# Performance work log

Measured on AMD Instinct MI355X. Metric: run time of the kernel, lower is better.

Reference implementation:

```python
import jax, jax.numpy as jnp
import numpy as np
from jax.scipy.special import logsumexp

B, T, K = 256, 512, 20
START_TAG, STOP_TAG = 18, 19


def setup_inputs() -> dict:
    key = jax.random.key(0)
    k1, k2, k3, k4 = jax.random.split(key, 4)
    features = jax.random.normal(k1, (B, T, K, K), dtype=jnp.float32)
    transitions = jax.random.normal(k2, (K, K), dtype=jnp.float32)
    targets = jax.random.randint(k3, (B, T), 0, 18, dtype=jnp.int32)
    lengths = jax.random.randint(k4, (B,), 1, T + 1, dtype=jnp.int32)
    return {"features": features, "transitions": transitions,
            "targets": targets, "lengths": lengths}


def reference(features, transitions, targets, lengths):
    # features: [B, T, K, K] with features[b,t,i,j] = emission(tag i at t) + transition(j -> i)
    b, t, k, _ = features.shape
    valid = jnp.arange(t)[None, :] < lengths[:, None]  # [B, T]

    # ---- gold path score ----
    prev = jnp.concatenate(
        [jnp.full((b, 1), START_TAG, dtype=targets.dtype), targets[:, :-1]], axis=1)
    flat_idx = targets.astype(jnp.int32) * k + prev.astype(jnp.int32)  # [B, T]
    scores_at_targets = jnp.take_along_axis(
        features.reshape(b, t, k * k), flat_idx[:, :, None].astype(jnp.int32), axis=2)[..., 0]
    last_tag = jnp.take_along_axis(targets, (lengths - 1)[:, None].astype(jnp.int32), axis=1)[:, 0]
    gold_score = jnp.sum(jnp.where(valid, scores_at_targets, 0.0)) \
        + jnp.sum(transitions[STOP_TAG, last_tag])

    # ---- forward algorithm (sequential log-sum-exp scan over time) ----
    alpha0 = features[:, 0, :, START_TAG]  # [B, K]; all lengths >= 1

    def step(alpha, inp):
        f_t, tt = inp  # f_t: [B, K, K]
        new = logsumexp(f_t + alpha[:, None, :], axis=2)  # [B, K]
        active = (tt < lengths)[:, None]
        return jnp.where(active, new, alpha), None

    feats_rest = jnp.swapaxes(features[:, 1:], 0, 1)  # [T-1, B, K, K]
    alpha, _ = jax.lax.scan(step, alpha0, (feats_rest, jnp.arange(1, t)))

    all_paths_scores = jnp.sum(logsumexp(alpha + transitions[STOP_TAG][None, :], axis=1))
    return all_paths_scores - gold_score
```

## Files before the change

kernel.cpp:

```cpp
#include <hip/hip_runtime.h>
#include <math.h>
#include <stdint.h>

#define BB 256
#define TT 512
#define KK 20
#define START_TAG 18
#define STOP_TAG 19
#define NST 400
#define SEGSTRIDE 420
#define WS_SEG_OFF 1024

typedef __bf16 bf16x8 __attribute__((ext_vector_type(8)));
typedef float f32x16 __attribute__((ext_vector_type(16)));
typedef uint32_t u32x4 __attribute__((ext_vector_type(4)));

__device__ __forceinline__ float fexp2(float x){ float r; asm("v_exp_f32 %0, %1":"=v"(r):"v"(x)); return r; }
__device__ __forceinline__ float flog2(float x){ float r; asm("v_log_f32 %0, %1":"=v"(r):"v"(x)); return r; }
__device__ __forceinline__ uint32_t pk_bf16(float lo, float hi){
  uint32_t r; asm("v_cvt_pk_bf16_f32 %0, %1, %2":"=v"(r):"v"(lo),"v"(hi)); return r;
}
__device__ __forceinline__ void pswap(uint32_t &a, uint32_t &b){
  asm("v_permlane32_swap_b32 %0, %1":"+v"(a),"+v"(b));
}
__device__ __forceinline__ f32x16 mfma_bf16(u32x4 a, u32x4 b, f32x16 c){
  return __builtin_amdgcn_mfma_f32_32x32x16_bf16(
    __builtin_bit_cast(bf16x8,a), __builtin_bit_cast(bf16x8,b), c, 0,0,0);
}

template<int SEGL, int SEGS>
__global__ __launch_bounds__(64) void seg_mfma(
    const float* __restrict__ feats, const int* __restrict__ lengths,
    float* __restrict__ wseg)
{
  constexpr float LOG2E = 1.4426950408889634f;
  const int lane = threadIdx.x;
  const int n  = lane & 31;
  const int hi = lane >> 5;
  const int task = blockIdx.x;
  const int b = task / SEGS;
  const int s = task - b*SEGS;
  const int seg0 = 1 + SEGL*s;
  const int len = lengths[b];
  int nv = len - seg0; nv = nv < 0 ? 0 : (nv > SEGL ? SEGL : nv);
  if (nv <= 0) return;

  const bool rowok = n < KK;
  const int rli = rowok ? n : 0;
  const float* rbase = feats + (size_t)(b*TT + seg0)*NST + rli*KK;
  const int off0 = hi ? 8 : 0;

  u32x4 B0, B1;
  #pragma unroll
  for (int d=0; d<4; ++d){
    int k0 = hi*8 + 2*d;
    uint32_t v = 0;
    if (k0   == n && n < KK) v |= 0x3F80u;
    if (k0+1 == n && n < KK) v |= 0x3F800000u;
    B0[d] = v;
    int m0 = 16 + hi*8 + 2*d;
    uint32_t u = 0;
    if (m0   == n && n < KK) u |= 0x3F800000u * 0 + ((m0 == n && n < KK) ? 0x3F80u : 0u);
    u = 0;
    if (m0   == n && n < KK) u |= 0x3F80u;
    if (m0+1 == n && n < KK) u |= 0x3F800000u;
    B1[d] = u;
  }

  int cexp = 0;
  f32x16 acc;
  #pragma unroll
  for (int r=0;r<16;++r) acc[r] = 0.f;

  float4 a0,a1,a2, p0,p1,p2, q0,q1,q2;
  auto LD = [&](int it, float4 &r0, float4 &r1, float4 &r2){
    const float* p = rbase + (size_t)it*NST;
    r0 = *(const float4*)(p + off0);
    r1 = *(const float4*)(p + off0 + 4);
    r2 = (hi == 0) ? *(const float4*)(p + 16) : make_float4(0.f,0.f,0.f,0.f);
  };
  auto CONV = [&](const float4 &r0, const float4 &r1, const float4 &r2,
                  u32x4 &A0, u32x4 &A1){
    uint32_t w0 = pk_bf16(fexp2(r0.x*LOG2E), fexp2(r0.y*LOG2E));
    uint32_t w1 = pk_bf16(fexp2(r0.z*LOG2E), fexp2(r0.w*LOG2E));
    uint32_t w2 = pk_bf16(fexp2(r1.x*LOG2E), fexp2(r1.y*LOG2E));
    uint32_t w3 = pk_bf16(fexp2(r1.z*LOG2E), fexp2(r1.w*LOG2E));
    uint32_t w4 = pk_bf16(fexp2(r2.x*LOG2E), fexp2(r2.y*LOG2E));
    uint32_t w5 = pk_bf16(fexp2(r2.z*LOG2E), fexp2(r2.w*LOG2E));
    if (!rowok){ w0=0u; w1=0u; w2=0u; w3=0u; }
    if (!(rowok && hi==0)){ w4=0u; w5=0u; }
    A0[0]=w0; A0[1]=w1; A0[2]=w2; A0[3]=w3;
    A1[0]=w4; A1[1]=w5; A1[2]=0u; A1[3]=0u;
  };
  auto RENORM = [&](){
    float mx = acc[0];
    #pragma unroll
    for (int r=1;r<16;++r) mx = fmaxf(mx, acc[r]);
    mx = fmaxf(mx, __shfl_xor(mx, 32, 64));
    int e = (int)((__float_as_uint(mx) >> 23) & 255) - 127;
    if (e < -100) e = -100;
    float sc = __uint_as_float((uint32_t)(127 - e) << 23);
    #pragma unroll
    for (int r=0;r<16;++r) acc[r] *= sc;
    cexp += e;
  };
  auto C2B = [&](){
    uint32_t x0 = pk_bf16(acc[0],  acc[1]);
    uint32_t x1 = pk_bf16(acc[2],  acc[3]);
    uint32_t x2 = pk_bf16(acc[4],  acc[5]);
    uint32_t x3 = pk_bf16(acc[6],  acc[7]);
    uint32_t x4 = pk_bf16(acc[8],  acc[9]);
    uint32_t x5 = pk_bf16(acc[10], acc[11]);
    uint32_t x6 = pk_bf16(acc[12], acc[13]);
    uint32_t x7 = pk_bf16(acc[14], acc[15]);
    pswap(x0,x2); pswap(x1,x3); pswap(x4,x6); pswap(x5,x7);
    B0[0]=x0; B0[1]=x1; B0[2]=x2; B0[3]=x3;
    B1[0]=x4; B1[1]=x5; B1[2]=x6; B1[3]=x7;
  };

  LD(0, a0,a1,a2);
  LD((1 < nv) ? 1 : 0, p0,p1,p2);
  q0=a0; q1=a1; q2=a2;
  for (int it=0; it<nv; ++it){
    if (it+2 < nv) LD(it+2, q0,q1,q2);
    u32x4 A0, A1; CONV(a0,a1,a2, A0,A1);
    f32x16 z;
    #pragma unroll
    for (int r=0;r<16;++r) z[r] = 0.f;
    acc = mfma_bf16(A0, B0, z);
    acc = mfma_bf16(A1, B1, acc);
    if (it == nv-1) break;
    if ((it & 7) == 7) RENORM();
    C2B();
    a0=p0; a1=p1; a2=p2;
    p0=q0; p1=q1; p2=q2;
  }
  RENORM();

  float* out = wseg + (size_t)task*SEGSTRIDE;
  #pragma unroll
  for (int r=0;r<16;++r){
    int row = (r&3) + 8*(r>>2) + 4*hi;
    if (row < KK && n < KK) out[row*KK + n] = acc[r];
  }
  if (hi==0 && n<KK) ((int*)out)[NST + n] = cexp;
}

template<int SEGL, int SEGS>
__global__ __launch_bounds__(64,1) void chain_kernel2(
    const float* __restrict__ feats, const float* __restrict__ trans,
    const int* __restrict__ targets, const int* __restrict__ lengths,
    const float* __restrict__ wseg, float* __restrict__ partialA)
{
    constexpr float LOG2E = 1.4426950408889634f;
    constexpr float LN2   = 0.6931471805599453f;
    const int b = blockIdx.x;
    const int lane = threadIdx.x;
    const int len = lengths[b];
    const bool act = lane < KK;
    const int li = act ? lane : 0;

    __shared__ __align__(16) float Ul[KK];

    const float* fb = feats + (size_t)b*TT*NST;
    float a2 = fb[li*KK + START_TAG] * LOG2E;
    float c0 = __uint_as_float(__builtin_amdgcn_readfirstlane(__float_as_uint(a2)));
    float CW = c0;
    float wk = act ? fexp2(a2 - c0) : 0.f;

    const int nseg = (len - 1 + SEGL - 1) / SEGL;

    if (act && nseg > 0){
        float4 mA[5], mB[5];
        int cA = 0, cB = 0;
        auto LDM = [&](int s2, float4 (&m)[5], int& c){
            const float* base = wseg + (size_t)(b*SEGS + s2)*SEGSTRIDE;
            const float4* p4 = (const float4*)(base + li*KK);
            m[0]=p4[0]; m[1]=p4[1]; m[2]=p4[2]; m[3]=p4[3]; m[4]=p4[4];
            c = ((const int*)base)[NST + li];
        };
        auto STEP = [&](float4 (&m)[5], int c){
            int e = (int)((__float_as_uint(wk) >> 23) & 255) - 127;
            int q = __builtin_amdgcn_readfirstlane(c + e);
            Ul[li] = ldexpf(wk, c - q);
            asm volatile("s_waitcnt lgkmcnt(0)" ::: "memory");
            const float4* up = (const float4*)Ul;
            float4 u0 = up[0], u1 = up[1], u2 = up[2], u3 = up[3], u4 = up[4];
            float s0 = m[0].x*u0.x, s1 = m[0].y*u0.y;
            s0 = fmaf(m[0].z,u0.z,s0); s1 = fmaf(m[0].w,u0.w,s1);
            s0 = fmaf(m[1].x,u1.x,s0); s1 = fmaf(m[1].y,u1.y,s1);
            s0 = fmaf(m[1].z,u1.z,s0); s1 = fmaf(m[1].w,u1.w,s1);
            s0 = fmaf(m[2].x,u2.x,s0); s1 = fmaf(m[2].y,u2.y,s1);
            s0 = fmaf(m[2].z,u2.z,s0); s1 = fmaf(m[2].w,u2.w,s1);
            s0 = fmaf(m[3].x,u3.x,s0); s1 = fmaf(m[3].y,u3.y,s1);
            s0 = fmaf(m[3].z,u3.z,s0); s1 = fmaf(m[3].w,u3.w,s1);
            s0 = fmaf(m[4].x,u4.x,s0); s1 = fmaf(m[4].y,u4.y,s1);
            s0 = fmaf(m[4].z,u4.z,s0); s1 = fmaf(m[4].w,u4.w,s1);
            wk = s0 + s1;
            CW += (float)q;
            asm volatile("s_waitcnt lgkmcnt(0)" ::: "memory");
        };
        LDM(0, mA, cA);
        for (int s2 = 0; s2 < nseg; ){
            if (s2 + 1 < nseg) LDM(s2 + 1, mB, cB);
            STEP(mA, cA);
            ++s2; if (s2 >= nseg) break;
            if (s2 + 1 < nseg) LDM(s2 + 1, mA, cA);
            STEP(mB, cB);
            ++s2;
        }
    }

    float term = act ? wk * fexp2(trans[STOP_TAG*KK + li] * LOG2E) : 0.f;
    #pragma unroll
    for (int o = 32; o > 0; o >>= 1) term += __shfl_xor(term, o, 64);
    if (lane == 0){
        float lse = LN2 * (CW + flog2(term));
        int last = targets[b*TT + len - 1];
        partialA[b] = lse - trans[STOP_TAG*KK + last];
    }
}

__global__ __launch_bounds__(64,1) void fwd_serial(
    const float* __restrict__ feats, const float* __restrict__ trans,
    const int* __restrict__ targets, const int* __restrict__ lengths,
    float* __restrict__ partialA)
{
    constexpr float LOG2E = 1.4426950408889634f;
    constexpr float LN2   = 0.6931471805599453f;
    const int b    = blockIdx.x;
    const int lane = threadIdx.x;
    const int len  = lengths[b];
    const float* fb = feats + (size_t)b * TT * NST;
    __shared__ __align__(16) float alpha[KK];
    __shared__ __align__(16) float xs[KK];
    const bool act = lane < KK;
    const int  li  = act ? lane : 0;
    if (act) alpha[lane] = fb[lane * KK + START_TAG] * LOG2E;
    __syncthreads();
    float4 b0[5], b1[5], b2[5], b3[5];
    auto LOAD = [&](float4* dst, int t){
        int tc = (t < len) ? t : (len - 1);
        const float4* p = (const float4*)(fb + (size_t)tc * NST + li * KK);
        dst[0]=p[0]; dst[1]=p[1]; dst[2]=p[2]; dst[3]=p[3]; dst[4]=p[4];
    };
    auto STEP = [&](const float4* bufv){
        const float4* ap = (const float4*)alpha;
        float a[KK];
        #pragma unroll
        for (int q = 0; q < 5; ++q){
            float4 av = ap[q];
            a[4*q+0]=av.x; a[4*q+1]=av.y; a[4*q+2]=av.z; a[4*q+3]=av.w;
        }
        float v[KK];
        #pragma unroll
        for (int q = 0; q < 5; ++q){
            v[4*q+0] = bufv[q].x * LOG2E + a[4*q+0];
            v[4*q+1] = bufv[q].y * LOG2E + a[4*q+1];
            v[4*q+2] = bufv[q].z * LOG2E + a[4*q+2];
            v[4*q+3] = bufv[q].w * LOG2E + a[4*q+3];
        }
        float m = v[0];
        #pragma unroll
        for (int j = 1; j < KK; ++j) m = fmaxf(m, v[j]);
        float s = 0.f;
        #pragma unroll
        for (int j = 0; j < KK; ++j) s += fexp2(v[j] - m);
        float na = m + flog2(s);
        __syncthreads();
        if (act) alpha[lane] = na;
        __syncthreads();
    };
    LOAD(b0,1); LOAD(b1,2); LOAD(b2,3); LOAD(b3,4);
    int t = 1;
    while (t < len){
        STEP(b0); LOAD(b0, t+4); ++t; if (t >= len) break;
        STEP(b1); LOAD(b1, t+4); ++t; if (t >= len) break;
        STEP(b2); LOAD(b2, t+4); ++t; if (t >= len) break;
        STEP(b3); LOAD(b3, t+4); ++t;
    }
    if (act) xs[lane] = alpha[lane] + trans[STOP_TAG*KK + lane] * LOG2E;
    __syncthreads();
    if (lane == 0){
        float m = xs[0];
        for (int j = 1; j < KK; ++j) m = fmaxf(m, xs[j]);
        float s = 0.f;
        for (int j = 0; j < KK; ++j) s += fexp2(xs[j] - m);
        float lse = LN2 * (m + flog2(s));
        int last_tag = targets[b*TT + (len-1)];
        partialA[b] = lse - trans[STOP_TAG*KK + last_tag];
    }
}

__global__ __launch_bounds__(256) void gold_kernel(
    const float* __restrict__ feats, const int* __restrict__ targets,
    const int* __restrict__ lengths, float* __restrict__ partialG)
{
    const int b   = blockIdx.x;
    const int tt  = blockIdx.y * 256 + threadIdx.x;
    const int len = lengths[b];
    float val = 0.f;
    if (tt < len){
        int tgt  = targets[b*TT + tt];
        int prev = (tt > 0) ? targets[b*TT + tt - 1] : START_TAG;
        val = feats[((size_t)b*TT + tt)*NST + tgt*KK + prev];
    }
    #pragma unroll
    for (int off = 32; off > 0; off >>= 1) val += __shfl_down(val, off);
    __shared__ float wsum[4];
    if ((threadIdx.x & 63) == 0) wsum[threadIdx.x >> 6] = val;
    __syncthreads();
    if (threadIdx.x == 0)
        partialG[b*gridDim.y + blockIdx.y] = wsum[0]+wsum[1]+wsum[2]+wsum[3];
}

__global__ __launch_bounds__(256) void final_kernel(
    const float* __restrict__ partialA, const float* __restrict__ partialG,
    float* __restrict__ out)
{
    int tid = threadIdx.x;
    float v = partialA[tid] - partialG[tid] - partialG[tid + 256];
    #pragma unroll
    for (int off = 32; off > 0; off >>= 1) v += __shfl_down(v, off);
    __shared__ float wsum[4];
    if ((tid & 63) == 0) wsum[tid >> 6] = v;
    __syncthreads();
    if (tid == 0) out[0] = wsum[0]+wsum[1]+wsum[2]+wsum[3];
}

extern "C" void kernel_launch(void* const* d_in, const int* in_sizes, int n_in,
                              void* d_out, int out_size, void* d_ws, size_t ws_size,
                              hipStream_t stream) {
    const float* feats   = (const float*)d_in[0];
    const float* trans   = (const float*)d_in[1];
    const int*   targets = (const int*)d_in[2];
    const int*   lengths = (const int*)d_in[3];

    float* ws       = (float*)d_ws;
    float* partialA = ws;
    float* partialG = ws + 256;
    float* wseg     = ws + WS_SEG_OFF;

    const size_t need64 = (size_t)(WS_SEG_OFF + (size_t)BB*8*SEGSTRIDE) * sizeof(float);

    if (ws_size >= need64){
        seg_mfma<64,8><<<dim3(BB*8), dim3(64), 0, stream>>>(feats, lengths, wseg);
        chain_kernel2<64,8><<<dim3(BB), dim3(64), 0, stream>>>(feats, trans, targets, lengths, wseg, partialA);
    } else {
        fwd_serial<<<dim3(BB), dim3(64), 0, stream>>>(feats, trans, targets, lengths, partialA);
    }
    gold_kernel<<<dim3(BB, 2), dim3(256), 0, stream>>>(feats, targets, lengths, partialG);
    final_kernel<<<dim3(1), dim3(256), 0, stream>>>(partialA, partialG, (float*)d_out);
}
```

Before: 48.83 us.

## Fuse gold-path scoring into segment MFMA kernel and deepen load prefetch

The gold-path gather moves into seg_mfma, which already reads each feature row, so the separate gold_kernel pass over features is gone. Per-segment partial gold sums are written to partialG and reduced in a new templated final kernel. The t=0 gold term is added in chain_kernel2. The load pipeline also goes from a three-deep rotation to a four-deep manual unroll, at the cost of more registers, extra target loads and select logic per step.

```diff
diff --git a/kernel.cpp b/kernel.cpp
--- a/kernel.cpp
+++ b/kernel.cpp
@@ -9,7 +9,7 @@
 #define STOP_TAG 19
 #define NST 400
 #define SEGSTRIDE 420
-#define WS_SEG_OFF 1024
+#define WS_SEG_OFF 4096
 
 typedef __bf16 bf16x8 __attribute__((ext_vector_type(8)));
 typedef float f32x16 __attribute__((ext_vector_type(16)));
@@ -30,8 +30,9 @@
 
 template<int SEGL, int SEGS>
 __global__ __launch_bounds__(64) void seg_mfma(
-    const float* __restrict__ feats, const int* __restrict__ lengths,
-    float* __restrict__ wseg)
+    const float* __restrict__ feats, const int* __restrict__ targets,
+    const int* __restrict__ lengths, float* __restrict__ wseg,
+    float* __restrict__ partialG)
 {
   constexpr float LOG2E = 1.4426950408889634f;
   const int lane = threadIdx.x;
@@ -43,12 +44,13 @@
   const int seg0 = 1 + SEGL*s;
   const int len = lengths[b];
   int nv = len - seg0; nv = nv < 0 ? 0 : (nv > SEGL ? SEGL : nv);
-  if (nv <= 0) return;
+  if (nv <= 0){ if (lane == 0) partialG[task] = 0.f; return; }
 
   const bool rowok = n < KK;
   const int rli = rowok ? n : 0;
   const float* rbase = feats + (size_t)(b*TT + seg0)*NST + rli*KK;
   const int off0 = hi ? 8 : 0;
+  const int bT = b*TT;
 
   u32x4 B0, B1;
   #pragma unroll
@@ -60,27 +62,47 @@
     B0[d] = v;
     int m0 = 16 + hi*8 + 2*d;
     uint32_t u = 0;
-    if (m0   == n && n < KK) u |= 0x3F800000u * 0 + ((m0 == n && n < KK) ? 0x3F80u : 0u);
-    u = 0;
     if (m0   == n && n < KK) u |= 0x3F80u;
     if (m0+1 == n && n < KK) u |= 0x3F800000u;
     B1[d] = u;
   }
 
   int cexp = 0;
+  float gold = 0.f;
   f32x16 acc;
   #pragma unroll
   for (int r=0;r<16;++r) acc[r] = 0.f;
 
-  float4 a0,a1,a2, p0,p1,p2, q0,q1,q2;
-  auto LD = [&](int it, float4 &r0, float4 &r1, float4 &r2){
+  auto LDr = [&](int it, float4 &r0, float4 &r1, float4 &r2){
     const float* p = rbase + (size_t)it*NST;
     r0 = *(const float4*)(p + off0);
     r1 = *(const float4*)(p + off0 + 4);
     r2 = (hi == 0) ? *(const float4*)(p + 16) : make_float4(0.f,0.f,0.f,0.f);
   };
-  auto CONV = [&](const float4 &r0, const float4 &r1, const float4 &r2,
-                  u32x4 &A0, u32x4 &A1){
+
+  auto RENORM = [&](){
+    float mx = acc[0];
+    #pragma unroll
+    for (int r=1;r<16;++r) mx = fmaxf(mx, acc[r]);
+    mx = fmaxf(mx, __shfl_xor(mx, 32, 64));
+    int e = (int)((__float_as_uint(mx) >> 23) & 255) - 127;
+    if (e < -100) e = -100;
+    float sc = __uint_as_float((uint32_t)(127 - e) << 23);
+    #pragma unroll
+    for (int r=0;r<16;++r) acc[r] *= sc;
+    cexp += e;
+  };
+
+  auto BODY = [&](float4 &r0, float4 &r1, float4 &r2, int it){
+    int t   = seg0 + it;
+    int tgt = targets[bT + t];
+    int prv = targets[bT + t - 1];
+    int hsel = (prv >= 8 && prv < 16) ? 1 : 0;
+    int rsel = (prv >= 16) ? 2 : (((prv & 7) >= 4) ? 1 : 0);
+    int comp = prv & 3;
+    float4 rr = (rsel == 0) ? r0 : ((rsel == 1) ? r1 : r2);
+    float vv = (comp==0)?rr.x:((comp==1)?rr.y:((comp==2)?rr.z:rr.w));
+    if (n == tgt && hi == hsel) gold += vv;
     uint32_t w0 = pk_bf16(fexp2(r0.x*LOG2E), fexp2(r0.y*LOG2E));
     uint32_t w1 = pk_bf16(fexp2(r0.z*LOG2E), fexp2(r0.w*LOG2E));
     uint32_t w2 = pk_bf16(fexp2(r1.x*LOG2E), fexp2(r1.y*LOG2E));
@@ -89,51 +111,41 @@
     uint32_t w5 = pk_bf16(fexp2(r2.z*LOG2E), fexp2(r2.w*LOG2E));
     if (!rowok){ w0=0u; w1=0u; w2=0u; w3=0u; }
     if (!(rowok && hi==0)){ w4=0u; w5=0u; }
+    u32x4 A0, A1;
     A0[0]=w0; A0[1]=w1; A0[2]=w2; A0[3]=w3;
     A1[0]=w4; A1[1]=w5; A1[2]=0u; A1[3]=0u;
-  };
-  auto RENORM = [&](){
-    float mx = acc[0];
-    #pragma unroll
-    for (int r=1;r<16;++r) mx = fmaxf(mx, acc[r]);
-    mx = fmaxf(mx, __shfl_xor(mx, 32, 64));
-    int e = (int)((__float_as_uint(mx) >> 23) & 255) - 127;
-    if (e < -100) e = -100;
-    float sc = __uint_as_float((uint32_t)(127 - e) << 23);
-    #pragma unroll
-    for (int r=0;r<16;++r) acc[r] *= sc;
-    cexp += e;
-  };
-  auto C2B = [&](){
-    uint32_t x0 = pk_bf16(acc[0],  acc[1]);
-    uint32_t x1 = pk_bf16(acc[2],  acc[3]);
-    uint32_t x2 = pk_bf16(acc[4],  acc[5]);
-    uint32_t x3 = pk_bf16(acc[6],  acc[7]);
-    uint32_t x4 = pk_bf16(acc[8],  acc[9]);
-    uint32_t x5 = pk_bf16(acc[10], acc[11]);
-    uint32_t x6 = pk_bf16(acc[12], acc[13]);
-    uint32_t x7 = pk_bf16(acc[14], acc[15]);
-    pswap(x0,x2); pswap(x1,x3); pswap(x4,x6); pswap(x5,x7);
-    B0[0]=x0; B0[1]=x1; B0[2]=x2; B0[3]=x3;
-    B1[0]=x4; B1[1]=x5; B1[2]=x6; B1[3]=x7;
-  };
-
-  LD(0, a0,a1,a2);
-  LD((1 < nv) ? 1 : 0, p0,p1,p2);
-  q0=a0; q1=a1; q2=a2;
-  for (int it=0; it<nv; ++it){
-    if (it+2 < nv) LD(it+2, q0,q1,q2);
-    u32x4 A0, A1; CONV(a0,a1,a2, A0,A1);
     f32x16 z;
     #pragma unroll
     for (int r=0;r<16;++r) z[r] = 0.f;
     acc = mfma_bf16(A0, B0, z);
     acc = mfma_bf16(A1, B1, acc);
-    if (it == nv-1) break;
-    if ((it & 7) == 7) RENORM();
-    C2B();
-    a0=p0; a1=p1; a2=p2;
-    p0=q0; p1=q1; p2=q2;
+    if (it != nv-1){
+      if ((it & 7) == 7) RENORM();
+      uint32_t x0 = pk_bf16(acc[0],  acc[1]);
+      uint32_t x1 = pk_bf16(acc[2],  acc[3]);
+      uint32_t x2 = pk_bf16(acc[4],  acc[5]);
+      uint32_t x3 = pk_bf16(acc[6],  acc[7]);
+      uint32_t x4 = pk_bf16(acc[8],  acc[9]);
+      uint32_t x5 = pk_bf16(acc[10], acc[11]);
+      uint32_t x6 = pk_bf16(acc[12], acc[13]);
+      uint32_t x7 = pk_bf16(acc[14], acc[15]);
+      pswap(x0,x2); pswap(x1,x3); pswap(x4,x6); pswap(x5,x7);
+      B0[0]=x0; B0[1]=x1; B0[2]=x2; B0[3]=x3;
+      B1[0]=x4; B1[1]=x5; B1[2]=x6; B1[3]=x7;
+    }
+  };
+
+  float4 a0,a1,a2, b0,b1,b2, c0,c1,c2, d0,d1,d2;
+  LDr(0, a0,a1,a2);
+  if (1 < nv) LDr(1, b0,b1,b2);
+  if (2 < nv) LDr(2, c0,c1,c2);
+  if (3 < nv) LDr(3, d0,d1,d2);
+  int it = 0;
+  while (true){
+    BODY(a0,a1,a2, it); if (it+4 < nv) LDr(it+4, a0,a1,a2); if (++it >= nv) break;
+    BODY(b0,b1,b2, it); if (it+4 < nv) LDr(it+4, b0,b1,b2); if (++it >= nv) break;
+    BODY(c0,c1,c2, it); if (it+4 < nv) LDr(it+4, c0,c1,c2); if (++it >= nv) break;
+    BODY(d0,d1,d2, it); if (it+4 < nv) LDr(it+4, d0,d1,d2); if (++it >= nv) break;
   }
   RENORM();
 
@@ -144,6 +156,10 @@
     if (row < KK && n < KK) out[row*KK + n] = acc[r];
   }
   if (hi==0 && n<KK) ((int*)out)[NST + n] = cexp;
+
+  #pragma unroll
+  for (int o = 32; o > 0; o >>= 1) gold += __shfl_xor(gold, o, 64);
+  if (lane == 0) partialG[task] = gold;
 }
 
 template<int SEGL, int SEGS>
@@ -217,8 +233,27 @@
     if (lane == 0){
         float lse = LN2 * (CW + flog2(term));
         int last = targets[b*TT + len - 1];
-        partialA[b] = lse - trans[STOP_TAG*KK + last];
-    }
+        float g0 = fb[targets[b*TT]*KK + START_TAG];
+        partialA[b] = lse - trans[STOP_TAG*KK + last] - g0;
+    }
+}
+
+template<int SEGS>
+__global__ __launch_bounds__(256) void final_kernel(
+    const float* __restrict__ partialA, const float* __restrict__ partialG,
+    float* __restrict__ out)
+{
+    int tid = threadIdx.x;
+    float g = 0.f;
+    #pragma unroll
+    for (int k = 0; k < SEGS; ++k) g += partialG[tid*SEGS + k];
+    float v = partialA[tid] - g;
+    #pragma unroll
+    for (int off = 32; off > 0; off >>= 1) v += __shfl_down(v, off);
+    __shared__ float wsum[4];
+    if ((tid & 63) == 0) wsum[tid >> 6] = v;
+    __syncthreads();
+    if (tid == 0) out[0] = wsum[0]+wsum[1]+wsum[2]+wsum[3];
 }
 
 __global__ __launch_bounds__(64,1) void fwd_serial(
@@ -314,7 +349,7 @@
         partialG[b*gridDim.y + blockIdx.y] = wsum[0]+wsum[1]+wsum[2]+wsum[3];
 }
 
-__global__ __launch_bounds__(256) void final_kernel(
+__global__ __launch_bounds__(256) void final_fb(
     const float* __restrict__ partialA, const float* __restrict__ partialG,
     float* __restrict__ out)
 {
@@ -344,11 +379,12 @@
     const size_t need64 = (size_t)(WS_SEG_OFF + (size_t)BB*8*SEGSTRIDE) * sizeof(float);
 
     if (ws_size >= need64){
-        seg_mfma<64,8><<<dim3(BB*8), dim3(64), 0, stream>>>(feats, lengths, wseg);
+        seg_mfma<64,8><<<dim3(BB*8), dim3(64), 0, stream>>>(feats, targets, lengths, wseg, partialG);
         chain_kernel2<64,8><<<dim3(BB), dim3(64), 0, stream>>>(feats, trans, targets, lengths, wseg, partialA);
+        final_kernel<8><<<dim3(1), dim3(256), 0, stream>>>(partialA, partialG, (float*)d_out);
     } else {
         fwd_serial<<<dim3(BB), dim3(64), 0, stream>>>(feats, trans, targets, lengths, partialA);
-    }
-    gold_kernel<<<dim3(BB, 2), dim3(256), 0, stream>>>(feats, targets, lengths, partialG);
-    final_kernel<<<dim3(1), dim3(256), 0, stream>>>(partialA, partialG, (float*)d_out);
-}
+        gold_kernel<<<dim3(BB, 2), dim3(256), 0, stream>>>(feats, targets, lengths, partialG);
+        final_fb<<<dim3(1), dim3(256), 0, stream>>>(partialA, partialG, (float*)d_out);
+    }
+}
```

Result: no change. 49.05 us, median of 5 (+0.4%).
